# Kernel tuning notes

Measured on AMD Instinct MI355X. Metric: run time of the kernel, lower is better.

The kernel has to match this reference:

```python
import jax, jax.numpy as jnp
import numpy as np
from jax import lax

B, T, V, H = 32, 512, 4096, 1024


def _lstm_layer(x_proj, W_hh, b_hh):
    # x_proj: [B, T, 4H] = input-to-hidden projection (+ b_ih) precomputed for all steps
    h0 = jnp.zeros((x_proj.shape[0], H), x_proj.dtype)
    c0 = jnp.zeros_like(h0)

    def step(carry, xp_t):  # xp_t: [B, 4H]
        h, c = carry
        g = xp_t + h @ W_hh.T + b_hh
        i = jax.nn.sigmoid(g[:, :H])
        f = jax.nn.sigmoid(g[:, H:2 * H])
        gg = jnp.tanh(g[:, 2 * H:3 * H])
        o = jax.nn.sigmoid(g[:, 3 * H:])
        c = f * c + i * gg
        h = o * jnp.tanh(c)
        return (h, c), h

    _, hs = lax.scan(step, (h0, c0), x_proj.transpose(1, 0, 2))  # [T, B, H]
    return hs.transpose(1, 0, 2)  # [B, T, H]


def setup_inputs() -> dict:
    key = jax.random.key(0)
    ks = jax.random.split(key, 12)
    s_in = 1.0 / np.sqrt(H)
    u = lambda k, shape: jax.random.uniform(k, shape, jnp.float32, -s_in, s_in)
    return {
        "x": jax.random.randint(ks[0], (B, T), 0, V),
        "W_ih_l0": u(ks[1], (4 * H, V)),
        "W_hh_l0": u(ks[2], (4 * H, H)),
        "b_ih_l0": u(ks[3], (4 * H,)),
        "b_hh_l0": u(ks[4], (4 * H,)),
        "W_ih_l1": u(ks[5], (4 * H, H)),
        "W_hh_l1": u(ks[6], (4 * H, H)),
        "b_ih_l1": u(ks[7], (4 * H,)),
        "b_hh_l1": u(ks[8], (4 * H,)),
        "Wph": jax.random.normal(ks[9], (H, V), jnp.float32) * np.sqrt(2.0 / H),
        "bp": jnp.zeros((V,), jnp.float32),
    }


def reference(x, W_ih_l0, W_hh_l0, b_ih_l0, b_hh_l0,
              W_ih_l1, W_hh_l1, b_ih_l1, b_hh_l1, Wph, bp):
    # one_hot(x, V) @ W_ih_l0.T is mathematically a row-gather from W_ih_l0.T
    xp0 = jnp.take(W_ih_l0.T, x, axis=0) + b_ih_l0          # [B, T, 4H]
    h1 = _lstm_layer(xp0, W_hh_l0, b_hh_l0)                  # [B, T, H]
    xp1 = jnp.einsum('bth,gh->btg', h1, W_ih_l1) + b_ih_l1   # [B, T, 4H]
    h2 = _lstm_layer(xp1, W_hh_l1, b_hh_l1)                  # [B, T, H]
    return h2 @ Wph + bp                                     # [B, T, V]
```

## Files before the change

### kernel.cpp

```cpp
#include <hip/hip_runtime.h>
#include <cstdint>

typedef short bf16x8 __attribute__((ext_vector_type(8)));
typedef float f32x4 __attribute__((ext_vector_type(4)));
typedef unsigned u32x2 __attribute__((ext_vector_type(2)));
typedef int i32x2 __attribute__((ext_vector_type(2)));

__device__ __forceinline__ unsigned short f2bf(float f){
  unsigned u = __float_as_uint(f);
  u = u + 0x7fffu + ((u >> 16) & 1u);
  return (unsigned short)(u >> 16);
}
__device__ __forceinline__ float bf2f(unsigned short h){
  return __uint_as_float(((unsigned)h) << 16);
}

__device__ __forceinline__ void gld_lds16(const void* g, void* l){
  __builtin_amdgcn_global_load_lds((const __attribute__((address_space(1))) unsigned*)g,
                                   (__attribute__((address_space(3))) unsigned*)l, 16, 0, 0);
}

__device__ __forceinline__ i32x2 gload8i_cc_wait(const void* p){
  i32x2 r;
  asm volatile("global_load_dwordx2 %0, %1, off sc0 sc1\n\ts_waitcnt vmcnt(0)"
               : "=v"(r) : "v"(p) : "memory");
  return r;
}
__device__ __forceinline__ void gstore8_cc(void* p, u32x2 v){
  asm volatile("global_store_dwordx2 %0, %1, off sc0 sc1" :: "v"(p), "v"(v) : "memory");
}
__device__ __forceinline__ void wait_vm0(){
  asm volatile("s_waitcnt vmcnt(0)" ::: "memory");
  __builtin_amdgcn_sched_barrier(0);
}

__device__ __forceinline__ void pollwait(const int* f, int t, int lane){
  for (;;){
    i32x2 v = gload8i_cc_wait(f + lane * 2);
    if (__all(v.x >= t && v.y >= t)) break;
    __builtin_amdgcn_s_sleep(2);
  }
}

__global__ __launch_bounds__(256)
void k_cast(const float* __restrict__ in, unsigned short* __restrict__ out, int n){
  int i = (blockIdx.x * 256 + threadIdx.x) * 4;
  if (i + 3 < n){
    float4 v = *(const float4*)(in + i);
    ushort4 u;
    u.x = f2bf(v.x); u.y = f2bf(v.y); u.z = f2bf(v.z); u.w = f2bf(v.w);
    *(ushort4*)(out + i) = u;
  }
}

__global__ __launch_bounds__(256)
void k_cast2(const float* __restrict__ in, unsigned short* __restrict__ out, int coloff){
  int i = (blockIdx.x * 256 + threadIdx.x) * 4;
  if (i + 3 < 4194304){
    float4 v = *(const float4*)(in + i);
    ushort4 u;
    u.x = f2bf(v.x); u.y = f2bf(v.y); u.z = f2bf(v.z); u.w = f2bf(v.w);
    int r = i >> 10, c = i & 1023;
    *(ushort4*)(out + (size_t)r * 2048 + coloff + c) = u;
  }
}

__global__ __launch_bounds__(256)
void k_transpose_cast(const float* __restrict__ in, unsigned short* __restrict__ out,
                      int R, int C){
  __shared__ float tile[32][33];
  int tpr = C >> 5;
  int r0 = (blockIdx.x / tpr) * 32, c0 = (blockIdx.x % tpr) * 32;
  int lc = threadIdx.x & 31, lr = threadIdx.x >> 5;
  #pragma unroll
  for (int it = 0; it < 4; ++it)
    tile[lr + it*8][lc] = in[(size_t)(r0 + lr + it*8) * C + c0 + lc];
  __syncthreads();
  #pragma unroll
  for (int it = 0; it < 4; ++it){
    int oc = lr + it*8;
    out[(size_t)(c0 + oc) * R + r0 + lc] = f2bf(tile[lc][oc]);
  }
}

__global__ __launch_bounds__(256)
void k_gather(const unsigned short* __restrict__ Wt0, const int* __restrict__ x,
              unsigned short* __restrict__ xp){
  __shared__ unsigned short tile[32][520];
  __shared__ int tok[32];
  const int tid = threadIdx.x;
  const int t = blockIdx.x >> 3, rbase = (blockIdx.x & 7) * 512;
  if (tid < 32) tok[tid] = x[tid * 512 + t];
  __syncthreads();
  for (int b = 0; b < 32; ++b){
    unsigned v = *(const unsigned*)(Wt0 + (size_t)tok[b] * 4096 + rbase + tid * 2);
    *(unsigned*)&tile[b][tid * 2] = v;
  }
  __syncthreads();
  #pragma unroll
  for (int i = 0; i < 2; ++i){
    int rl = tid + i * 256;
    unsigned short vals[32];
    #pragma unroll
    for (int b = 0; b < 32; ++b) vals[b] = tile[b][rl];
    char* dst = (char*)xp + ((size_t)t * 131072 + (size_t)(rbase + rl) * 32) * 2;
    #pragma unroll
    for (int q = 0; q < 4; ++q){
      uint4 w;
      w.x = (unsigned)vals[q*8+0] | ((unsigned)vals[q*8+1] << 16);
      w.y = (unsigned)vals[q*8+2] | ((unsigned)vals[q*8+3] << 16);
      w.z = (unsigned)vals[q*8+4] | ((unsigned)vals[q*8+5] << 16);
      w.w = (unsigned)vals[q*8+6] | ((unsigned)vals[q*8+7] << 16);
      *(uint4*)(dst + q * 16) = w;
    }
  }
}

template<int L1R>
__device__ __forceinline__ void run_lstm5(
    const unsigned short* __restrict__ Wb,
    const unsigned short* __restrict__ xp,
    const float* __restrict__ b_ih, const float* __restrict__ b_hh,
    unsigned short* __restrict__ h_self,
    const unsigned short* __restrict__ h_in,
    int* __restrict__ flag_self, const int* __restrict__ flag_in,
    int jslot, char* lds)
{
  constexpr int KE  = L1R ? 2048 : 1024;
  constexpr int RS  = KE * 2;
  constexpr int KB2 = KE / 64;

  const int tid = threadIdx.x, lane = tid & 63, wv = tid >> 6;
  const int wv_k = wv & 1, wv_b = (wv >> 1) & 1, wv_m = wv >> 2;
  const int l15 = lane & 15, l4 = (lane >> 4) & 3;
  const int jbase = jslot * 8;

  bf16x8 afr[KB2];
  {
    const int ar = wv_m * 16 + l15;
    const int grow = (ar >> 3) * 1024 + jbase + (ar & 7);
    const char* wrow = (const char*)Wb + (size_t)grow * RS + wv_k * KE + l4 * 16;
    #pragma unroll
    for (int i = 0; i < KB2; ++i) afr[i] = *(const bf16x8*)(wrow + i * 64);
  }

  const int ab = tid >> 3, aj = tid & 7;
  const int jb = jbase + aj;
  float bi = 0.f, bff = 0.f, bg = 0.f, bo = 0.f;
  if (tid < 256){
    bi  = b_ih[jb]        + b_hh[jb];
    bff = b_ih[1024 + jb] + b_hh[1024 + jb];
    bg  = b_ih[2048 + jb] + b_hh[2048 + jb];
    bo  = b_ih[3072 + jb] + b_hh[3072 + jb];
  }
  float c = 0.f;
  float* gl = (float*)lds;
  const int brow = wv_b * 16 + l15;
  const int bswz = (brow & 7) << 4;
  const size_t bbase = (size_t)brow * RS;
  const int kofs0 = wv_k * KE + l4 * 16;
  const f32x4 zero = {0.f, 0.f, 0.f, 0.f};

  for (int t = 0; t < 512; ++t){
    float xr0 = 0.f, xr1 = 0.f, xr2 = 0.f, xr3 = 0.f;
    if (!L1R && wv_k == 0){
      const unsigned short* xpt = xp + (size_t)t * 131072 + wv_b * 16 + l15;
      int sr = wv_m * 16 + l4 * 4;
      int g0 = ((sr + 0) >> 3) * 1024 + jbase + ((sr + 0) & 7);
      int g1 = ((sr + 1) >> 3) * 1024 + jbase + ((sr + 1) & 7);
      int g2 = ((sr + 2) >> 3) * 1024 + jbase + ((sr + 2) & 7);
      int g3 = ((sr + 3) >> 3) * 1024 + jbase + ((sr + 3) & 7);
      xr0 = bf2f(xpt[(size_t)g0 * 32]);
      xr1 = bf2f(xpt[(size_t)g1 * 32]);
      xr2 = bf2f(xpt[(size_t)g2 * 32]);
      xr3 = bf2f(xpt[(size_t)g3 * 32]);
    }

    if (wv == 0){
      if (L1R){
        pollwait(flag_in,   t,     lane);
        pollwait(flag_self, t - 1, lane);
      } else {
        pollwait(flag_in,   t - 1, lane);
      }
    }
    __syncthreads();

    if (!L1R){
      if (t == 0){
        #pragma unroll
        for (int it = 0; it < 8; ++it)
          *(f32x4*)(lds + it * 8192 + tid * 16) = zero;
      } else {
        const char* hp = (const char*)h_self + (size_t)(t - 1) * 65536;
        #pragma unroll
        for (int it = 0; it < 8; ++it){
          int u = it * 8192 + tid * 16;
          int b = u >> 11, kb = u & 2047;
          gld_lds16(hp + (size_t)b * 2048 + (kb ^ ((b & 7) << 4)), lds + u);
        }
      }
    } else {
      const char* hA = (const char*)h_in + (size_t)t * 65536;
      #pragma unroll
      for (int it = 0; it < 8; ++it){
        int u = it * 8192 + tid * 16;
        int b = u >> 11, kb = u & 2047;
        gld_lds16(hA + (size_t)b * 2048 + (kb ^ ((b & 7) << 4)), lds + (size_t)b * 4096 + kb);
      }
      if (t == 0){
        #pragma unroll
        for (int it = 0; it < 8; ++it){
          int u = it * 8192 + tid * 16;
          int b = u >> 11, kb = u & 2047;
          *(f32x4*)(lds + (size_t)b * 4096 + 2048 + kb) = zero;
        }
      } else {
        const char* hB = (const char*)h_self + (size_t)(t - 1) * 65536;
        #pragma unroll
        for (int it = 0; it < 8; ++it){
          int u = it * 8192 + tid * 16;
          int b = u >> 11, kb = u & 2047;
          gld_lds16(hB + (size_t)b * 2048 + (kb ^ ((b & 7) << 4)), lds + (size_t)b * 4096 + 2048 + kb);
        }
      }
    }
    __syncthreads();

    f32x4 a0 = zero, a1 = zero, a2 = zero, a3 = zero;
    if (!L1R && wv_k == 0){ a0[0] = xr0; a0[1] = xr1; a0[2] = xr2; a0[3] = xr3; }
    #pragma unroll
    for (int i = 0; i < KB2; i += 4){
      bf16x8 b0 = *(const bf16x8*)(lds + bbase + (((i + 0) * 64 + kofs0) ^ bswz));
      bf16x8 b1 = *(const bf16x8*)(lds + bbase + (((i + 1) * 64 + kofs0) ^ bswz));
      bf16x8 b2 = *(const bf16x8*)(lds + bbase + (((i + 2) * 64 + kofs0) ^ bswz));
      bf16x8 b3 = *(const bf16x8*)(lds + bbase + (((i + 3) * 64 + kofs0) ^ bswz));
      a0 = __builtin_amdgcn_mfma_f32_16x16x32_bf16(afr[i + 0], b0, a0, 0, 0, 0);
      a1 = __builtin_amdgcn_mfma_f32_16x16x32_bf16(afr[i + 1], b1, a1, 0, 0, 0);
      a2 = __builtin_amdgcn_mfma_f32_16x16x32_bf16(afr[i + 2], b2, a2, 0, 0, 0);
      a3 = __builtin_amdgcn_mfma_f32_16x16x32_bf16(afr[i + 3], b3, a3, 0, 0, 0);
    }
    a0 += a1; a2 += a3; a0 += a2;
    __syncthreads();

    {
      int srow = wv_m * 16 + l4 * 4;
      float* g = gl + wv_k * 1056 + srow * 33 + wv_b * 16 + l15;
      g[0] = a0[0]; g[33] = a0[1]; g[66] = a0[2]; g[99] = a0[3];
    }
    __syncthreads();

    if (tid < 256){
      float gi = gl[aj * 33 + ab]          + gl[1056 + aj * 33 + ab]          + bi;
      float gf = gl[(8 + aj) * 33 + ab]    + gl[1056 + (8 + aj) * 33 + ab]    + bff;
      float gg = gl[(16 + aj) * 33 + ab]   + gl[1056 + (16 + aj) * 33 + ab]   + bg;
      float go = gl[(24 + aj) * 33 + ab]   + gl[1056 + (24 + aj) * 33 + ab]   + bo;
      float i_ = 1.f / (1.f + __expf(-gi));
      float f_ = 1.f / (1.f + __expf(-gf));
      float g_ = 1.f - 2.f / (1.f + __expf(2.f * gg));
      float o_ = 1.f / (1.f + __expf(-go));
      c = f_ * c + i_ * g_;
      float h_ = o_ * (1.f - 2.f / (1.f + __expf(2.f * c)));
      unsigned p = (unsigned)f2bf(h_);
      unsigned w = p | (((unsigned)__shfl_xor((int)p, 1) & 0xFFFFu) << 16);
      unsigned d1 = (unsigned)__shfl_xor((int)w, 2);
      if ((aj & 3) == 0){
        u32x2 W2; W2.x = w; W2.y = d1;
        gstore8_cc((char*)h_self + (size_t)t * 65536 + (size_t)ab * 2048 + (size_t)(jbase + aj) * 2, W2);
      }
    }
    wait_vm0();
    __syncthreads();
    if (tid == 0)
      __hip_atomic_store(flag_self + jslot, t, __ATOMIC_RELAXED, __HIP_MEMORY_SCOPE_AGENT);
  }
}

__global__ __launch_bounds__(512, 1)
void k_fused(const unsigned short* __restrict__ Whh0b,
             const unsigned short* __restrict__ Wcat1,
             const unsigned short* __restrict__ xp,
             const float* __restrict__ bih0, const float* __restrict__ bhh0,
             const float* __restrict__ bih1, const float* __restrict__ bhh1,
             unsigned short* __restrict__ h1seq, unsigned short* __restrict__ h2seq,
             int* __restrict__ flag0, int* __restrict__ flag1)
{
  __shared__ char lds[131072];
  __threadfence();
  const int bid = blockIdx.x;
  if (bid < 128)
    run_lstm5<0>(Whh0b, xp, bih0, bhh0, h1seq, nullptr, flag0, flag0, bid, lds);
  else
    run_lstm5<1>(Wcat1, nullptr, bih1, bhh1, h2seq, h1seq, flag1, flag0, bid - 128, lds);
}

__global__ __launch_bounds__(256, 2)
void k_gemm(const unsigned short* __restrict__ A,
            const unsigned short* __restrict__ B,
            int Mtiles, void* __restrict__ outp,
            const float* __restrict__ bp, int mode)
{
  __shared__ char As[16384];
  __shared__ char Bs[16384];
  const int tid = threadIdx.x, lane = tid & 63, wv = tid >> 6;
  const int mq = (wv >> 1) * 64, nq = (wv & 1) * 64;
  const int l15 = lane & 15, l4 = (lane >> 4) & 3;
  const int mt = blockIdx.x % Mtiles, nt = blockIdx.x / Mtiles;
  const char* Abase = (const char*)A + (size_t)(mt * 128) * 2048;
  const char* Bbase = (const char*)B + (size_t)(nt * 128) * 2048;
  const f32x4 zero = {0.f, 0.f, 0.f, 0.f};
  f32x4 acc[4][4];
  #pragma unroll
  for (int i = 0; i < 4; ++i)
    #pragma unroll
    for (int j = 0; j < 4; ++j) acc[i][j] = zero;

  for (int kt = 0; kt < 16; ++kt){
    __syncthreads();
    #pragma unroll
    for (int p = 0; p < 4; ++p){
      int o = p * 4096 + tid * 16;
      int row = o >> 7, kb = o & 127;
      gld_lds16(Abase + (size_t)row * 2048 + kt * 128 + (kb ^ ((row & 7) << 4)), As + o);
    }
    #pragma unroll
    for (int p = 0; p < 4; ++p){
      int o = p * 4096 + tid * 16;
      int row = o >> 7, kb = o & 127;
      gld_lds16(Bbase + (size_t)row * 2048 + kt * 128 + (kb ^ ((row & 7) << 4)), Bs + o);
    }
    __syncthreads();
    #pragma unroll
    for (int kk = 0; kk < 2; ++kk){
      bf16x8 af[4], bfr[4];
      #pragma unroll
      for (int i = 0; i < 4; ++i){
        int row = mq + i * 16 + l15;
        int kbyte = kk * 64 + l4 * 16;
        af[i]  = *(const bf16x8*)(As + row * 128 + (kbyte ^ ((row & 7) << 4)));
        int nrow = nq + i * 16 + l15;
        bfr[i] = *(const bf16x8*)(Bs + nrow * 128 + (kbyte ^ ((nrow & 7) << 4)));
      }
      #pragma unroll
      for (int i = 0; i < 4; ++i)
        #pragma unroll
        for (int j = 0; j < 4; ++j)
          acc[i][j] = __builtin_amdgcn_mfma_f32_16x16x32_bf16(af[i], bfr[j], acc[i][j], 0, 0, 0);
    }
  }

  if (mode == 0){
    unsigned short* o16 = (unsigned short*)outp;
    #pragma unroll
    for (int i = 0; i < 4; ++i)
      #pragma unroll
      for (int j = 0; j < 4; ++j){
        int n = nt * 128 + nq + j * 16 + l15;
        int tt = n >> 5, bc = n & 31;
        #pragma unroll
        for (int r = 0; r < 4; ++r){
          int m = mt * 128 + mq + i * 16 + l4 * 4 + r;
          o16[(size_t)tt * 131072 + (size_t)m * 32 + bc] = f2bf(acc[i][j][r]);
        }
      }
  } else {
    float* of = (float*)outp;
    #pragma unroll
    for (int j = 0; j < 4; ++j){
      int v = nt * 128 + nq + j * 16 + l15;
      float bias = bp[v];
      #pragma unroll
      for (int i = 0; i < 4; ++i)
        #pragma unroll
        for (int r = 0; r < 4; ++r){
          int tb = mt * 128 + mq + i * 16 + l4 * 4 + r;
          int tt = tb >> 5, bb2 = tb & 31;
          of[(size_t)bb2 * 2097152 + (size_t)tt * 4096 + v] = acc[i][j][r] + bias;
        }
    }
  }
}

extern "C" void kernel_launch(void* const* d_in, const int* in_sizes, int n_in,
                              void* d_out, int out_size, void* d_ws, size_t ws_size,
                              hipStream_t stream)
{
  const int*   x    = (const int*)  d_in[0];
  const float* Wih0 = (const float*)d_in[1];
  const float* Whh0 = (const float*)d_in[2];
  const float* bih0 = (const float*)d_in[3];
  const float* bhh0 = (const float*)d_in[4];
  const float* Wih1 = (const float*)d_in[5];
  const float* Whh1 = (const float*)d_in[6];
  const float* bih1 = (const float*)d_in[7];
  const float* bhh1 = (const float*)d_in[8];
  const float* Wph  = (const float*)d_in[9];
  const float* bp   = (const float*)d_in[10];

  char* ws = (char*)d_ws;
  int* flag0 = (int*)ws;
  int* flag1 = (int*)(ws + 512);
  unsigned short* Whh0b = (unsigned short*)(ws + 4096);
  char* regA = ws + 4096 + 8388608;
  unsigned short* Wt0   = (unsigned short*)regA;
  unsigned short* Wcat1 = (unsigned short*)regA;
  unsigned short* WphT  = (unsigned short*)(regA + 16777216);
  unsigned short* h1seq = (unsigned short*)(ws + 4096 + 8388608 + 33554432);
  unsigned short* h2seq = (unsigned short*)(ws + 4096 + 8388608 + 33554432 + 33554432);
  unsigned short* xpbuf = (unsigned short*)d_out;

  hipMemsetAsync(d_ws, 0xFF, 1024, stream);

  k_transpose_cast<<<16384, 256, 0, stream>>>(Wih0, Wt0, 4096, 4096);
  k_gather<<<4096, 256, 0, stream>>>(Wt0, x, xpbuf);
  k_cast<<<4096, 256, 0, stream>>>(Whh0, Whh0b, 4194304);
  k_cast2<<<4096, 256, 0, stream>>>(Wih1, Wcat1, 0);
  k_cast2<<<4096, 256, 0, stream>>>(Whh1, Wcat1, 1024);
  k_transpose_cast<<<4096, 256, 0, stream>>>(Wph, WphT, 1024, 4096);

  k_fused<<<256, 512, 0, stream>>>(Whh0b, Wcat1, xpbuf, bih0, bhh0, bih1, bhh1,
                                   h1seq, h2seq, flag0, flag1);

  k_gemm<<<4096, 256, 0, stream>>>(h2seq, WphT, 128, d_out, bp, 1);
}
```

Measured before the change: 2.704 ms.

## Split recurrent MFMA work into four K-quarters per wave and merge flag polling

The per-step recurrent matmul is repartitioned so each of the eight waves covers one M half and one K quarter, computing both batch halves and reusing each weight fragment across two MFMAs. Partial sums from four K groups are reduced in LDS, and the x-projection is now read directly by the gate threads instead of being injected into the accumulator. Layer-1 polling issues both flag loads together, and the poll sleep interval is shortened. This is meant to shorten the per-step critical path and synchronization latency, at the cost of a larger LDS reduction and more frequent memory polling.

```diff
diff --git a/kernel.cpp b/kernel.cpp
--- a/kernel.cpp
+++ b/kernel.cpp
@@ -35,10 +35,24 @@
 }
 
 __device__ __forceinline__ void pollwait(const int* f, int t, int lane){
+  const int* p = f + lane * 2;
   for (;;){
-    i32x2 v = gload8i_cc_wait(f + lane * 2);
+    i32x2 v = gload8i_cc_wait(p);
     if (__all(v.x >= t && v.y >= t)) break;
-    __builtin_amdgcn_s_sleep(2);
+    __builtin_amdgcn_s_sleep(1);
+  }
+}
+__device__ __forceinline__ void pollwait2(const int* fA, int tA, const int* fB, int tB, int lane){
+  const int* pa = fA + lane * 2;
+  const int* pb = fB + lane * 2;
+  for (;;){
+    i32x2 a, b;
+    asm volatile("global_load_dwordx2 %0, %2, off sc0 sc1\n\t"
+                 "global_load_dwordx2 %1, %3, off sc0 sc1\n\t"
+                 "s_waitcnt vmcnt(0)"
+                 : "=&v"(a), "=&v"(b) : "v"(pa), "v"(pb) : "memory");
+    if (__all(a.x >= tA && a.y >= tA && b.x >= tB && b.y >= tB)) break;
+    __builtin_amdgcn_s_sleep(1);
   }
 }
 
@@ -117,7 +131,7 @@
 }
 
 template<int L1R>
-__device__ __forceinline__ void run_lstm5(
+__device__ __forceinline__ void run_lstm6(
     const unsigned short* __restrict__ Wb,
     const unsigned short* __restrict__ xp,
     const float* __restrict__ b_ih, const float* __restrict__ b_hh,
@@ -126,22 +140,22 @@
     int* __restrict__ flag_self, const int* __restrict__ flag_in,
     int jslot, char* lds)
 {
-  constexpr int KE  = L1R ? 2048 : 1024;
-  constexpr int RS  = KE * 2;
-  constexpr int KB2 = KE / 64;
+  constexpr int KE = L1R ? 2048 : 1024;
+  constexpr int RS = KE * 2;
+  constexpr int KS = KE / 128;
 
   const int tid = threadIdx.x, lane = tid & 63, wv = tid >> 6;
-  const int wv_k = wv & 1, wv_b = (wv >> 1) & 1, wv_m = wv >> 2;
+  const int wv_m = wv & 1, wv_q = wv >> 1;
   const int l15 = lane & 15, l4 = (lane >> 4) & 3;
   const int jbase = jslot * 8;
 
-  bf16x8 afr[KB2];
+  bf16x8 afr[KS];
   {
     const int ar = wv_m * 16 + l15;
     const int grow = (ar >> 3) * 1024 + jbase + (ar & 7);
-    const char* wrow = (const char*)Wb + (size_t)grow * RS + wv_k * KE + l4 * 16;
-    #pragma unroll
-    for (int i = 0; i < KB2; ++i) afr[i] = *(const bf16x8*)(wrow + i * 64);
+    const char* wrow = (const char*)Wb + (size_t)grow * RS + wv_q * (RS / 4) + l4 * 16;
+    #pragma unroll
+    for (int i = 0; i < KS; ++i) afr[i] = *(const bf16x8*)(wrow + i * 64);
   }
 
   const int ab = tid >> 3, aj = tid & 7;
@@ -155,34 +169,25 @@
   }
   float c = 0.f;
   float* gl = (float*)lds;
-  const int brow = wv_b * 16 + l15;
-  const int bswz = (brow & 7) << 4;
-  const size_t bbase = (size_t)brow * RS;
-  const int kofs0 = wv_k * KE + l4 * 16;
+  const int qoffB = wv_q * (RS / 4);
+  const int swz  = (l15 & 7) << 4;
+  const size_t row0 = (size_t)l15 * RS;
+  const size_t row1 = (size_t)(16 + l15) * RS;
   const f32x4 zero = {0.f, 0.f, 0.f, 0.f};
 
   for (int t = 0; t < 512; ++t){
     float xr0 = 0.f, xr1 = 0.f, xr2 = 0.f, xr3 = 0.f;
-    if (!L1R && wv_k == 0){
-      const unsigned short* xpt = xp + (size_t)t * 131072 + wv_b * 16 + l15;
-      int sr = wv_m * 16 + l4 * 4;
-      int g0 = ((sr + 0) >> 3) * 1024 + jbase + ((sr + 0) & 7);
-      int g1 = ((sr + 1) >> 3) * 1024 + jbase + ((sr + 1) & 7);
-      int g2 = ((sr + 2) >> 3) * 1024 + jbase + ((sr + 2) & 7);
-      int g3 = ((sr + 3) >> 3) * 1024 + jbase + ((sr + 3) & 7);
-      xr0 = bf2f(xpt[(size_t)g0 * 32]);
-      xr1 = bf2f(xpt[(size_t)g1 * 32]);
-      xr2 = bf2f(xpt[(size_t)g2 * 32]);
-      xr3 = bf2f(xpt[(size_t)g3 * 32]);
+    if (!L1R && tid < 256){
+      const unsigned short* xpt = xp + (size_t)t * 131072;
+      xr0 = bf2f(xpt[(size_t)jb * 32 + ab]);
+      xr1 = bf2f(xpt[(size_t)(1024 + jb) * 32 + ab]);
+      xr2 = bf2f(xpt[(size_t)(2048 + jb) * 32 + ab]);
+      xr3 = bf2f(xpt[(size_t)(3072 + jb) * 32 + ab]);
     }
 
     if (wv == 0){
-      if (L1R){
-        pollwait(flag_in,   t,     lane);
-        pollwait(flag_self, t - 1, lane);
-      } else {
-        pollwait(flag_in,   t - 1, lane);
-      }
+      if (L1R) pollwait2(flag_in, t, flag_self, t - 1, lane);
+      else     pollwait(flag_in, t - 1, lane);
     }
     __syncthreads();
 
@@ -227,34 +232,44 @@
     }
     __syncthreads();
 
-    f32x4 a0 = zero, a1 = zero, a2 = zero, a3 = zero;
-    if (!L1R && wv_k == 0){ a0[0] = xr0; a0[1] = xr1; a0[2] = xr2; a0[3] = xr3; }
-    #pragma unroll
-    for (int i = 0; i < KB2; i += 4){
-      bf16x8 b0 = *(const bf16x8*)(lds + bbase + (((i + 0) * 64 + kofs0) ^ bswz));
-      bf16x8 b1 = *(const bf16x8*)(lds + bbase + (((i + 1) * 64 + kofs0) ^ bswz));
-      bf16x8 b2 = *(const bf16x8*)(lds + bbase + (((i + 2) * 64 + kofs0) ^ bswz));
-      bf16x8 b3 = *(const bf16x8*)(lds + bbase + (((i + 3) * 64 + kofs0) ^ bswz));
-      a0 = __builtin_amdgcn_mfma_f32_16x16x32_bf16(afr[i + 0], b0, a0, 0, 0, 0);
-      a1 = __builtin_amdgcn_mfma_f32_16x16x32_bf16(afr[i + 1], b1, a1, 0, 0, 0);
-      a2 = __builtin_amdgcn_mfma_f32_16x16x32_bf16(afr[i + 2], b2, a2, 0, 0, 0);
-      a3 = __builtin_amdgcn_mfma_f32_16x16x32_bf16(afr[i + 3], b3, a3, 0, 0, 0);
-    }
-    a0 += a1; a2 += a3; a0 += a2;
+    f32x4 aA0 = zero, aA1 = zero, aB0 = zero, aB1 = zero;
+    #pragma unroll
+    for (int i = 0; i < KS; i += 2){
+      int o0 = (qoffB + (i + 0) * 64 + l4 * 16) ^ swz;
+      int o1 = (qoffB + (i + 1) * 64 + l4 * 16) ^ swz;
+      bf16x8 bA0 = *(const bf16x8*)(lds + row0 + o0);
+      bf16x8 bB0 = *(const bf16x8*)(lds + row1 + o0);
+      bf16x8 bA1 = *(const bf16x8*)(lds + row0 + o1);
+      bf16x8 bB1 = *(const bf16x8*)(lds + row1 + o1);
+      aA0 = __builtin_amdgcn_mfma_f32_16x16x32_bf16(afr[i],     bA0, aA0, 0, 0, 0);
+      aB0 = __builtin_amdgcn_mfma_f32_16x16x32_bf16(afr[i],     bB0, aB0, 0, 0, 0);
+      aA1 = __builtin_amdgcn_mfma_f32_16x16x32_bf16(afr[i + 1], bA1, aA1, 0, 0, 0);
+      aB1 = __builtin_amdgcn_mfma_f32_16x16x32_bf16(afr[i + 1], bB1, aB1, 0, 0, 0);
+    }
+    aA0 += aA1; aB0 += aB1;
     __syncthreads();
 
     {
-      int srow = wv_m * 16 + l4 * 4;
-      float* g = gl + wv_k * 1056 + srow * 33 + wv_b * 16 + l15;
-      g[0] = a0[0]; g[33] = a0[1]; g[66] = a0[2]; g[99] = a0[3];
+      float* g = gl + wv_q * 1056 + (wv_m * 16 + l4 * 4) * 33 + l15;
+      g[0]  = aA0[0]; g[33] = aA0[1]; g[66] = aA0[2]; g[99]  = aA0[3];
+      g[16] = aB0[0]; g[49] = aB0[1]; g[82] = aB0[2]; g[115] = aB0[3];
     }
     __syncthreads();
 
     if (tid < 256){
-      float gi = gl[aj * 33 + ab]          + gl[1056 + aj * 33 + ab]          + bi;
-      float gf = gl[(8 + aj) * 33 + ab]    + gl[1056 + (8 + aj) * 33 + ab]    + bff;
-      float gg = gl[(16 + aj) * 33 + ab]   + gl[1056 + (16 + aj) * 33 + ab]   + bg;
-      float go = gl[(24 + aj) * 33 + ab]   + gl[1056 + (24 + aj) * 33 + ab]   + bo;
+      float s0 = 0.f, s1 = 0.f, s2 = 0.f, s3 = 0.f;
+      #pragma unroll
+      for (int q = 0; q < 4; ++q){
+        const float* G = gl + q * 1056;
+        s0 += G[aj * 33 + ab];
+        s1 += G[(8 + aj) * 33 + ab];
+        s2 += G[(16 + aj) * 33 + ab];
+        s3 += G[(24 + aj) * 33 + ab];
+      }
+      float gi = s0 + xr0 + bi;
+      float gf = s1 + xr1 + bff;
+      float gg = s2 + xr2 + bg;
+      float go = s3 + xr3 + bo;
       float i_ = 1.f / (1.f + __expf(-gi));
       float f_ = 1.f / (1.f + __expf(-gf));
       float g_ = 1.f - 2.f / (1.f + __expf(2.f * gg));
@@ -289,9 +304,9 @@
   __threadfence();
   const int bid = blockIdx.x;
   if (bid < 128)
-    run_lstm5<0>(Whh0b, xp, bih0, bhh0, h1seq, nullptr, flag0, flag0, bid, lds);
+    run_lstm6<0>(Whh0b, xp, bih0, bhh0, h1seq, nullptr, flag0, flag0, bid, lds);
   else
-    run_lstm5<1>(Wcat1, nullptr, bih1, bhh1, h2seq, h1seq, flag1, flag0, bid - 128, lds);
+    run_lstm6<1>(Wcat1, nullptr, bih1, bhh1, h2seq, h1seq, flag1, flag0, bid - 128, lds);
 }
 
 __global__ __launch_bounds__(256, 2)
```

New measurement: 3.704 ms. 37.0% more time.

## Split recurrent LSTM blocks into two independent batch groups with separate flags

Applied to the files above, without the earlier changes.

Each layer's 128 blocks are split into two groups of 64 that each handle 16 batch rows. Every block now owns 16 hidden units instead of 8, so the per-step hidden-state load is halved and each group synchronises only on its own 64 flags, using single-dword polls. The input projection is added in the gate phase rather than seeded into the MFMA accumulator. This shrinks the cross-block dependency fan-in and per-step traffic, at the cost of more weight rows held in registers per block and a different flag layout that needs a larger memset.

```diff
diff --git a/kernel.cpp b/kernel.cpp
--- a/kernel.cpp
+++ b/kernel.cpp
@@ -4,7 +4,6 @@
 typedef short bf16x8 __attribute__((ext_vector_type(8)));
 typedef float f32x4 __attribute__((ext_vector_type(4)));
 typedef unsigned u32x2 __attribute__((ext_vector_type(2)));
-typedef int i32x2 __attribute__((ext_vector_type(2)));
 
 __device__ __forceinline__ unsigned short f2bf(float f){
   unsigned u = __float_as_uint(f);
@@ -20,12 +19,6 @@
                                    (__attribute__((address_space(3))) unsigned*)l, 16, 0, 0);
 }
 
-__device__ __forceinline__ i32x2 gload8i_cc_wait(const void* p){
-  i32x2 r;
-  asm volatile("global_load_dwordx2 %0, %1, off sc0 sc1\n\ts_waitcnt vmcnt(0)"
-               : "=v"(r) : "v"(p) : "memory");
-  return r;
-}
 __device__ __forceinline__ void gstore8_cc(void* p, u32x2 v){
   asm volatile("global_store_dwordx2 %0, %1, off sc0 sc1" :: "v"(p), "v"(v) : "memory");
 }
@@ -34,10 +27,13 @@
   __builtin_amdgcn_sched_barrier(0);
 }
 
-__device__ __forceinline__ void pollwait(const int* f, int t, int lane){
+__device__ __forceinline__ void pollwait64(const int* f, int t, int lane){
+  const int* p = f + lane;
   for (;;){
-    i32x2 v = gload8i_cc_wait(f + lane * 2);
-    if (__all(v.x >= t && v.y >= t)) break;
+    int v;
+    asm volatile("global_load_dword %0, %1, off sc0 sc1\n\ts_waitcnt vmcnt(0)"
+                 : "=v"(v) : "v"(p) : "memory");
+    if (__all(v >= t)) break;
     __builtin_amdgcn_s_sleep(2);
   }
 }
@@ -117,34 +113,33 @@
 }
 
 template<int L1R>
-__device__ __forceinline__ void run_lstm5(
+__device__ __forceinline__ void run_lstm8(
     const unsigned short* __restrict__ Wb,
     const unsigned short* __restrict__ xp,
     const float* __restrict__ b_ih, const float* __restrict__ b_hh,
     unsigned short* __restrict__ h_self,
     const unsigned short* __restrict__ h_in,
     int* __restrict__ flag_self, const int* __restrict__ flag_in,
-    int jslot, char* lds)
+    int jslot, int gbase, char* lds)
 {
   constexpr int KE  = L1R ? 2048 : 1024;
   constexpr int RS  = KE * 2;
   constexpr int KB2 = KE / 64;
 
   const int tid = threadIdx.x, lane = tid & 63, wv = tid >> 6;
-  const int wv_k = wv & 1, wv_b = (wv >> 1) & 1, wv_m = wv >> 2;
+  const int wv_k = wv & 1, wv_m = wv >> 1;
   const int l15 = lane & 15, l4 = (lane >> 4) & 3;
-  const int jbase = jslot * 8;
+  const int jbase = jslot * 16;
 
   bf16x8 afr[KB2];
   {
-    const int ar = wv_m * 16 + l15;
-    const int grow = (ar >> 3) * 1024 + jbase + (ar & 7);
+    const int grow = wv_m * 1024 + jbase + l15;
     const char* wrow = (const char*)Wb + (size_t)grow * RS + wv_k * KE + l4 * 16;
     #pragma unroll
     for (int i = 0; i < KB2; ++i) afr[i] = *(const bf16x8*)(wrow + i * 64);
   }
 
-  const int ab = tid >> 3, aj = tid & 7;
+  const int ab = tid >> 4, aj = tid & 15;
   const int jb = jbase + aj;
   float bi = 0.f, bff = 0.f, bg = 0.f, bo = 0.f;
   if (tid < 256){
@@ -155,33 +150,27 @@
   }
   float c = 0.f;
   float* gl = (float*)lds;
-  const int brow = wv_b * 16 + l15;
-  const int bswz = (brow & 7) << 4;
-  const size_t bbase = (size_t)brow * RS;
+  const size_t bbase = (size_t)l15 * RS;
+  const int bswz = (l15 & 7) << 4;
   const int kofs0 = wv_k * KE + l4 * 16;
   const f32x4 zero = {0.f, 0.f, 0.f, 0.f};
 
   for (int t = 0; t < 512; ++t){
     float xr0 = 0.f, xr1 = 0.f, xr2 = 0.f, xr3 = 0.f;
-    if (!L1R && wv_k == 0){
-      const unsigned short* xpt = xp + (size_t)t * 131072 + wv_b * 16 + l15;
-      int sr = wv_m * 16 + l4 * 4;
-      int g0 = ((sr + 0) >> 3) * 1024 + jbase + ((sr + 0) & 7);
-      int g1 = ((sr + 1) >> 3) * 1024 + jbase + ((sr + 1) & 7);
-      int g2 = ((sr + 2) >> 3) * 1024 + jbase + ((sr + 2) & 7);
-      int g3 = ((sr + 3) >> 3) * 1024 + jbase + ((sr + 3) & 7);
-      xr0 = bf2f(xpt[(size_t)g0 * 32]);
-      xr1 = bf2f(xpt[(size_t)g1 * 32]);
-      xr2 = bf2f(xpt[(size_t)g2 * 32]);
-      xr3 = bf2f(xpt[(size_t)g3 * 32]);
+    if (!L1R && tid < 256){
+      const unsigned short* xpt = xp + (size_t)t * 131072 + gbase + ab;
+      xr0 = bf2f(xpt[(size_t)jb * 32]);
+      xr1 = bf2f(xpt[(size_t)(1024 + jb) * 32]);
+      xr2 = bf2f(xpt[(size_t)(2048 + jb) * 32]);
+      xr3 = bf2f(xpt[(size_t)(3072 + jb) * 32]);
     }
 
     if (wv == 0){
       if (L1R){
-        pollwait(flag_in,   t,     lane);
-        pollwait(flag_self, t - 1, lane);
+        pollwait64(flag_in,   t,     lane);
+        pollwait64(flag_self, t - 1, lane);
       } else {
-        pollwait(flag_in,   t - 1, lane);
+        pollwait64(flag_in,   t - 1, lane);
       }
     }
     __syncthreads();
@@ -189,36 +178,36 @@
     if (!L1R){
       if (t == 0){
         #pragma unroll
-        for (int it = 0; it < 8; ++it)
+        for (int it = 0; it < 4; ++it)
           *(f32x4*)(lds + it * 8192 + tid * 16) = zero;
       } else {
-        const char* hp = (const char*)h_self + (size_t)(t - 1) * 65536;
-        #pragma unroll
-        for (int it = 0; it < 8; ++it){
+        const char* hp = (const char*)h_self + (size_t)(t - 1) * 65536 + (size_t)gbase * 2048;
+        #pragma unroll
+        for (int it = 0; it < 4; ++it){
           int u = it * 8192 + tid * 16;
           int b = u >> 11, kb = u & 2047;
           gld_lds16(hp + (size_t)b * 2048 + (kb ^ ((b & 7) << 4)), lds + u);
         }
       }
     } else {
-      const char* hA = (const char*)h_in + (size_t)t * 65536;
+      const char* hA = (const char*)h_in + (size_t)t * 65536 + (size_t)gbase * 2048;
       #pragma unroll
-      for (int it = 0; it < 8; ++it){
+      for (int it = 0; it < 4; ++it){
         int u = it * 8192 + tid * 16;
         int b = u >> 11, kb = u & 2047;
         gld_lds16(hA + (size_t)b * 2048 + (kb ^ ((b & 7) << 4)), lds + (size_t)b * 4096 + kb);
       }
       if (t == 0){
         #pragma unroll
-        for (int it = 0; it < 8; ++it){
+        for (int it = 0; it < 4; ++it){
           int u = it * 8192 + tid * 16;
           int b = u >> 11, kb = u & 2047;
           *(f32x4*)(lds + (size_t)b * 4096 + 2048 + kb) = zero;
         }
       } else {
-        const char* hB = (const char*)h_self + (size_t)(t - 1) * 65536;
-        #pragma unroll
-        for (int it = 0; it < 8; ++it){
+        const char* hB = (const char*)h_self + (size_t)(t - 1) * 65536 + (size_t)gbase * 2048;
+        #pragma unroll
+        for (int it = 0; it < 4; ++it){
           int u = it * 8192 + tid * 16;
           int b = u >> 11, kb = u & 2047;
           gld_lds16(hB + (size_t)b * 2048 + (kb ^ ((b & 7) << 4)), lds + (size_t)b * 4096 + 2048 + kb);
@@ -228,7 +217,6 @@
     __syncthreads();
 
     f32x4 a0 = zero, a1 = zero, a2 = zero, a3 = zero;
-    if (!L1R && wv_k == 0){ a0[0] = xr0; a0[1] = xr1; a0[2] = xr2; a0[3] = xr3; }
     #pragma unroll
     for (int i = 0; i < KB2; i += 4){
       bf16x8 b0 = *(const bf16x8*)(lds + bbase + (((i + 0) * 64 + kofs0) ^ bswz));
@@ -245,16 +233,16 @@
 
     {
       int srow = wv_m * 16 + l4 * 4;
-      float* g = gl + wv_k * 1056 + srow * 33 + wv_b * 16 + l15;
-      g[0] = a0[0]; g[33] = a0[1]; g[66] = a0[2]; g[99] = a0[3];
+      float* g = gl + wv_k * 1088 + srow * 17 + l15;
+      g[0] = a0[0]; g[17] = a0[1]; g[34] = a0[2]; g[51] = a0[3];
     }
     __syncthreads();
 
     if (tid < 256){
-      float gi = gl[aj * 33 + ab]          + gl[1056 + aj * 33 + ab]          + bi;
-      float gf = gl[(8 + aj) * 33 + ab]    + gl[1056 + (8 + aj) * 33 + ab]    + bff;
-      float gg = gl[(16 + aj) * 33 + ab]   + gl[1056 + (16 + aj) * 33 + ab]   + bg;
-      float go = gl[(24 + aj) * 33 + ab]   + gl[1056 + (24 + aj) * 33 + ab]   + bo;
+      float gi = gl[aj * 17 + ab]        + gl[1088 + aj * 17 + ab]        + xr0 + bi;
+      float gf = gl[(16 + aj) * 17 + ab] + gl[1088 + (16 + aj) * 17 + ab] + xr1 + bff;
+      float gg = gl[(32 + aj) * 17 + ab] + gl[1088 + (32 + aj) * 17 + ab] + xr2 + bg;
+      float go = gl[(48 + aj) * 17 + ab] + gl[1088 + (48 + aj) * 17 + ab] + xr3 + bo;
       float i_ = 1.f / (1.f + __expf(-gi));
       float f_ = 1.f / (1.f + __expf(-gf));
       float g_ = 1.f - 2.f / (1.f + __expf(2.f * gg));
@@ -266,7 +254,8 @@
       unsigned d1 = (unsigned)__shfl_xor((int)w, 2);
       if ((aj & 3) == 0){
         u32x2 W2; W2.x = w; W2.y = d1;
-        gstore8_cc((char*)h_self + (size_t)t * 65536 + (size_t)ab * 2048 + (size_t)(jbase + aj) * 2, W2);
+        gstore8_cc((char*)h_self + (size_t)t * 65536 + (size_t)(gbase + ab) * 2048
+                   + (size_t)(jbase + aj) * 2, W2);
       }
     }
     wait_vm0();
@@ -283,15 +272,22 @@
              const float* __restrict__ bih0, const float* __restrict__ bhh0,
              const float* __restrict__ bih1, const float* __restrict__ bhh1,
              unsigned short* __restrict__ h1seq, unsigned short* __restrict__ h2seq,
-             int* __restrict__ flag0, int* __restrict__ flag1)
+             int* __restrict__ flags)
 {
   __shared__ char lds[131072];
   __threadfence();
   const int bid = blockIdx.x;
-  if (bid < 128)
-    run_lstm5<0>(Whh0b, xp, bih0, bhh0, h1seq, nullptr, flag0, flag0, bid, lds);
+  const int layer = bid >> 7;
+  const int lbid  = bid & 127;
+  const int grp   = lbid >> 6;
+  const int jslot = lbid & 63;
+  const int gbase = grp * 16;
+  int* f0 = flags + grp * 128;
+  int* f1 = flags + 256 + grp * 128;
+  if (layer == 0)
+    run_lstm8<0>(Whh0b, xp, bih0, bhh0, h1seq, nullptr, f0, f0, jslot, gbase, lds);
   else
-    run_lstm5<1>(Wcat1, nullptr, bih1, bhh1, h2seq, h1seq, flag1, flag0, bid - 128, lds);
+    run_lstm8<1>(Wcat1, nullptr, bih1, bhh1, h2seq, h1seq, f1, f0, jslot, gbase, lds);
 }
 
 __global__ __launch_bounds__(256, 2)
@@ -398,8 +394,7 @@
   const float* bp   = (const float*)d_in[10];
 
   char* ws = (char*)d_ws;
-  int* flag0 = (int*)ws;
-  int* flag1 = (int*)(ws + 512);
+  int* flags = (int*)ws;
   unsigned short* Whh0b = (unsigned short*)(ws + 4096);
   char* regA = ws + 4096 + 8388608;
   unsigned short* Wt0   = (unsigned short*)regA;
@@ -409,7 +404,7 @@
   unsigned short* h2seq = (unsigned short*)(ws + 4096 + 8388608 + 33554432 + 33554432);
   unsigned short* xpbuf = (unsigned short*)d_out;
 
-  hipMemsetAsync(d_ws, 0xFF, 1024, stream);
+  hipMemsetAsync(d_ws, 0xFF, 2048, stream);
 
   k_transpose_cast<<<16384, 256, 0, stream>>>(Wih0, Wt0, 4096, 4096);
   k_gather<<<4096, 256, 0, stream>>>(Wt0, x, xpbuf);
@@ -419,7 +414,7 @@
   k_transpose_cast<<<4096, 256, 0, stream>>>(Wph, WphT, 1024, 4096);
 
   k_fused<<<256, 512, 0, stream>>>(Whh0b, Wcat1, xpbuf, bih0, bhh0, bih1, bhh1,
-                                   h1seq, h2seq, flag0, flag1);
+                                   h1seq, h2seq, flags);
 
   k_gemm<<<4096, 256, 0, stream>>>(h2seq, WphT, 128, d_out, bp, 1);
 }
```

Result: faster. 2.386 ms (-11.8%).
